# Kernel optimization log

Measured on AMD Instinct MI355X. Metric: run time of the kernel, lower is better.

## Reference

```python
import jax, jax.numpy as jnp
import numpy as np

B, T, D, H, L, V = 2, 1024, 1024, 16, 6, 32000
HD = D // H  # head_size = n_emb // n_heads
EPS = 1e-5   # torch LayerNorm default


def setup_inputs() -> dict:
    key = jax.random.key(0)
    ks = jax.random.split(key, 19)
    s = 0.02
    n = lambda k, shape: jax.random.normal(k, shape, dtype=jnp.float32) * s
    return {
        "idx": jax.random.randint(ks[0], (B, T), 0, V),
        "targets": jax.random.randint(ks[1], (B, T), 0, V),
        "tok_emb": n(ks[2], (V, D)),
        "pos_emb": n(ks[3], (V, D)),  # only first T rows used, as in the source
        "Wq": n(ks[4], (L, H, D, HD)),
        "Wk": n(ks[5], (L, H, D, HD)),
        "Wv": n(ks[6], (L, H, D, HD)),
        "Wo": n(ks[7], (L, D, D)),
        "bo": n(ks[8], (L, D)),
        "W1": n(ks[9], (L, D, 4 * D)),
        "b1": n(ks[10], (L, 4 * D)),
        "W2": n(ks[11], (L, 4 * D, D)),
        "b2": n(ks[12], (L, D)),
        "ln_g": jnp.ones((D,), jnp.float32),
        "ln_b": jnp.zeros((D,), jnp.float32),
        "Wf": n(ks[13], (D, V)),
        "bf": n(ks[14], (V,)),
    }


def _layer_norm(x, g, b):
    mu = jnp.mean(x, axis=-1, keepdims=True)
    var = jnp.mean(jnp.square(x - mu), axis=-1, keepdims=True)
    return (x - mu) * jax.lax.rsqrt(var + EPS) * g + b


def _forward(idx, targets, tok_emb, pos_emb, Wq, Wk, Wv, Wo, bo,
             W1, b1, W2, b2, ln_g, ln_b, Wf, bf):
    x = tok_emb[idx] + pos_emb[:T]  # [B,T,D]
    tril = jnp.tril(jnp.ones((T, T), dtype=bool))
    scale = jnp.asarray(D, x.dtype) ** -0.5  # NOTE: source scales by C=N_EMBED, not head_size

    def block(x, p):
        wq, wk, wv, wo, bo_, w1, b1_, w2, b2_ = p
        q = jnp.einsum('btd,hde->bhte', x, wq)
        k = jnp.einsum('btd,hde->bhte', x, wk)
        v = jnp.einsum('btd,hde->bhte', x, wv)
        scores = jnp.einsum('bhte,bhse->bhts', q, k) * scale
        scores = jnp.where(tril, scores, -jnp.inf)
        att = jax.nn.softmax(scores, axis=-1)
        o = jnp.einsum('bhts,bhse->bhte', att, v)
        o = o.transpose(0, 2, 1, 3).reshape(B, T, D)  # concat heads
        x = x + o @ wo + bo_                           # attn residual (no LN in source)
        h = jax.nn.relu(x @ w1 + b1_)
        x = x + h @ w2 + b2_                           # ffn residual
        return x, None

    x, _ = jax.lax.scan(block, x, (Wq, Wk, Wv, Wo, bo, W1, b1, W2, b2))
    x = _layer_norm(x, ln_g, ln_b)
    logits = x @ Wf + bf  # [B,T,V]
    logp = jax.nn.log_softmax(logits, axis=-1)
    nll = -jnp.take_along_axis(logp, targets[..., None], axis=-1)
    loss = jnp.mean(nll)
    return logits, loss


def reference(idx, targets, tok_emb, pos_emb, Wq, Wk, Wv, Wo, bo,
              W1, b1, W2, b2, ln_g, ln_b, Wf, bf):
    return _forward(idx, targets, tok_emb, pos_emb, Wq, Wk, Wv, Wo, bo,
                    W1, b1, W2, b2, ln_g, ln_b, Wf, bf)
```

## Files before the change

### kernel.cpp

```cpp
#include <hip/hip_runtime.h>
#include <hip/hip_bf16.h>

typedef unsigned short u16;
typedef unsigned int u32;
typedef float f32x4 __attribute__((ext_vector_type(4)));
typedef __bf16 bf16x8 __attribute__((ext_vector_type(8)));

#define NB 2
#define NT 1024
#define ND 1024
#define NH 16
#define HDIM 64
#define NL 6
#define NV 32000
#define ND4 4096
#define BT (NB * NT)
#define L2E 1.44269504f
#define NSLOT 500

__device__ __forceinline__ u16 f2b(float f) {
  u32 u = __builtin_bit_cast(u32, f);
  u32 r = (u + 0x7FFFu + ((u >> 16) & 1u)) >> 16;
  return (u16)r;
}

__device__ __forceinline__ void gl_lds16(const void* g, void* lds) {
  __builtin_amdgcn_global_load_lds((const __attribute__((address_space(1))) u32*)g,
                                   (__attribute__((address_space(3))) u32*)lds, 16, 0, 0);
}

__device__ __forceinline__ float rsum16(float v) {
  v += __shfl_xor(v, 1, 64);
  v += __shfl_xor(v, 2, 64);
  v += __shfl_xor(v, 4, 64);
  v += __shfl_xor(v, 8, 64);
  return v;
}

__device__ __forceinline__ void tr512(const float* in, int in_rs, u16* out, int out_rs,
                                      int k0, int n0, float (*t)[65]) {
  int tid = threadIdx.x;
#pragma unroll
  for (int i = 0; i < 8; ++i) {
    int e = tid + 512 * i;
    int r = e >> 6, c = e & 63;
    t[r][c] = in[(size_t)(k0 + r) * in_rs + n0 + c];
  }
  __syncthreads();
#pragma unroll
  for (int i = 0; i < 8; ++i) {
    int e = tid + 512 * i;
    int r = e >> 6, c = e & 63;
    out[(size_t)(n0 + r) * out_rs + k0 + c] = f2b(t[c][r]);
  }
}

__device__ __forceinline__ void trans512_blk(
    int i, int l, const float* Wq, const float* Wk, const float* Wv,
    const float* Wo, const float* W1, const float* W2,
    u16* wqkvT, u16* woT, u16* w1T, u16* w2T, float (*t)[65]) {
  if (i < 768) {
    int x = i & 15, z = i >> 4;
    int s = z >> 4, h = z & 15;
    const float* in = (s == 0 ? Wq : s == 1 ? Wk : Wv) + ((size_t)(l * NH + h)) * ND * HDIM;
    u16* o = wqkvT + ((size_t)(s * ND + h * HDIM)) * ND;
    tr512(in, HDIM, o, ND, x * 64, 0, t);
  } else if (i < 1024) {
    int j = i - 768, x = j & 15, y = j >> 4;
    tr512(Wo + (size_t)l * ND * ND, ND, woT, ND, y * 64, x * 64, t);
  } else if (i < 2048) {
    int j = i - 1024, x = j & 63, y = j >> 6;
    tr512(W1 + (size_t)l * ND * ND4, ND4, w1T, ND, y * 64, x * 64, t);
  } else {
    int j = i - 2048, x = j & 15, y = j >> 4;
    tr512(W2 + (size_t)l * ND4 * ND, ND, w2T, ND4, y * 64, x * 64, t);
  }
}

__global__ void __launch_bounds__(512) k_pre(const int* __restrict__ idx,
                                             const float* __restrict__ tok,
                                             const float* __restrict__ pos,
                                             float* __restrict__ xf, u16* __restrict__ xb,
                                             const float* __restrict__ Wq,
                                             const float* __restrict__ Wk,
                                             const float* __restrict__ Wv,
                                             const float* __restrict__ Wo,
                                             const float* __restrict__ W1,
                                             const float* __restrict__ W2,
                                             u16* __restrict__ wT0) {
  __shared__ float t[64][65];
  int bid = blockIdx.x;
  if (bid < 1024) {
    int tid = threadIdx.x;
    int row = bid * 2 + (tid >> 8);
    int tt = row & (NT - 1);
    int tk = idx[row];
    int c = (tid & 255) * 4;
    float4 a = *(const float4*)(tok + (size_t)tk * ND + c);
    float4 p = *(const float4*)(pos + (size_t)tt * ND + c);
    float4 s = make_float4(a.x + p.x, a.y + p.y, a.z + p.z, a.w + p.w);
    *(float4*)(xf + (size_t)row * ND + c) = s;
    u16* o = xb + (size_t)row * ND + c;
    *(u32*)(o + 0) = (u32)f2b(s.x) | ((u32)f2b(s.y) << 16);
    *(u32*)(o + 2) = (u32)f2b(s.z) | ((u32)f2b(s.w) << 16);
    return;
  }
  trans512_blk(bid - 1024, 0, Wq, Wk, Wv, Wo, W1, W2,
               wT0, wT0 + (size_t)3 * ND * ND, wT0 + (size_t)4 * ND * ND,
               wT0 + (size_t)8 * ND * ND, t);
}

template <int EPI>
__global__ void __launch_bounds__(512, 2)
k_gemm8(const u16* __restrict__ A, const u16* __restrict__ Bt,
        const float* __restrict__ bias, float* __restrict__ outf,
        u16* __restrict__ outb, int K, int N, int nMt, float* __restrict__ pl) {
  __shared__ u16 lds[2][2][2][128 * 64];
  int tid = threadIdx.x;
  int w = tid >> 6, l = tid & 63;
  int l4 = l >> 4, lm = l & 15;
  int wm = w >> 2, wn = w & 3;

  int nwg = gridDim.x, bid = blockIdx.x;
  int q8 = nwg >> 3, r8 = nwg & 7;
  int xcd = bid & 7, loc = bid >> 3;
  int swz = (xcd < r8 ? xcd * (q8 + 1) : r8 * (q8 + 1) + (xcd - r8) * q8) + loc;
  int m0 = (swz % nMt) * 256;
  int n0 = (swz / nMt) * 256;

  f32x4 acc[8][4];
  f32x4 z = {0.f, 0.f, 0.f, 0.f};
#pragma unroll
  for (int m = 0; m < 8; ++m)
#pragma unroll
    for (int n = 0; n < 4; ++n) acc[m][n] = z;

  int srow = (w << 3) + (l >> 3);
  int scol = (((l & 7) ^ ((l >> 3) & 7)) << 3);
  int sdst = w * 512 + l * 8;

  auto stage_half = [&](int b, int mat, int h, int kt) {
    int k0 = kt << 6;
    const u16* base = (mat == 0 ? A + (size_t)(m0 + (h << 7)) * K
                                : Bt + (size_t)(n0 + (h << 7)) * K);
#pragma unroll
    for (int i = 0; i < 2; ++i)
      gl_lds16(base + (size_t)(i * 64 + srow) * K + k0 + scol,
               &lds[b][mat][h][i * 4096 + sdst]);
  };

  int c0 = (l4 ^ (lm & 7)) * 8;
  int c1 = c0 ^ 32;
  int brow0 = (wn & 1) * 64;

  const u16* A0h = &lds[0][0][wm][0];
  const u16* B0h = &lds[0][1][wn >> 1][0];
  const u16* A1h = &lds[1][0][wm][0];
  const u16* B1h = &lds[1][1][wn >> 1][0];

  bf16x8 Ar[4][2], Bx[2][2], By[2][2];

  auto dsA = [&](const u16* Ah, int mf0) {
#pragma unroll
    for (int mf = 0; mf < 4; ++mf) {
      Ar[mf][0] = *(const bf16x8*)&Ah[((mf0 + mf) * 16 + lm) * 64 + c0];
      Ar[mf][1] = *(const bf16x8*)&Ah[((mf0 + mf) * 16 + lm) * 64 + c1];
    }
  };
  auto dsB = [&](const u16* Bh, bf16x8 (&B)[2][2], int nf0) {
#pragma unroll
    for (int nf = 0; nf < 2; ++nf) {
      B[nf][0] = *(const bf16x8*)&Bh[(brow0 + (nf0 + nf) * 16 + lm) * 64 + c0];
      B[nf][1] = *(const bf16x8*)&Bh[(brow0 + (nf0 + nf) * 16 + lm) * 64 + c1];
    }
  };
  auto mm = [&](int am, bf16x8 (&B)[2][2], int an) {
    __builtin_amdgcn_s_setprio(1);
#pragma unroll
    for (int mf = 0; mf < 4; ++mf)
#pragma unroll
      for (int nf = 0; nf < 2; ++nf) {
        acc[am + mf][an + nf] =
            __builtin_amdgcn_mfma_f32_16x16x32_bf16(Ar[mf][0], B[nf][0], acc[am + mf][an + nf], 0, 0, 0);
        acc[am + mf][an + nf] =
            __builtin_amdgcn_mfma_f32_16x16x32_bf16(Ar[mf][1], B[nf][1], acc[am + mf][an + nf], 0, 0, 0);
      }
    __builtin_amdgcn_s_setprio(0);
  };
  auto openbar = [&]() {
    __builtin_amdgcn_sched_barrier(0);
    __builtin_amdgcn_s_barrier();
    __builtin_amdgcn_sched_barrier(0);
  };
  auto midbar = [&]() {
    __builtin_amdgcn_sched_barrier(0);
    __builtin_amdgcn_s_barrier();
    asm volatile("s_waitcnt lgkmcnt(0)" ::: "memory");
    __builtin_amdgcn_sched_barrier(0);
  };

  int nk = K >> 6;
  stage_half(0, 0, 0, 0); stage_half(0, 0, 1, 0);
  stage_half(0, 1, 0, 0); stage_half(0, 1, 1, 0);
  stage_half(1, 0, 0, 1);

  for (int u = 0; u < nk; u += 2) {
    bool s2 = (u + 2 < nk), s3 = (u + 3 < nk);
    asm volatile("s_waitcnt vmcnt(2)" ::: "memory");
    openbar();
    dsA(A0h, 0); dsB(B0h, Bx, 0);
    stage_half(1, 0, 1, u + 1);
    midbar();
    mm(0, Bx, 0);
    openbar();
    dsB(B0h, By, 2);
    stage_half(1, 1, 0, u + 1);
    midbar();
    mm(0, By, 2);
    openbar();
    dsA(A0h, 4);
    stage_half(1, 1, 1, u + 1);
    midbar();
    mm(4, By, 2);
    openbar();
    if (s2) stage_half(0, 0, 0, u + 2);
    midbar();
    mm(4, Bx, 0);
    if (s2) asm volatile("s_waitcnt vmcnt(2)" ::: "memory");
    else    asm volatile("s_waitcnt vmcnt(0)" ::: "memory");
    openbar();
    dsA(A1h, 0); dsB(B1h, Bx, 0);
    if (s2) stage_half(0, 0, 1, u + 2);
    midbar();
    mm(0, Bx, 0);
    openbar();
    dsB(B1h, By, 2);
    if (s2) stage_half(0, 1, 0, u + 2);
    midbar();
    mm(0, By, 2);
    openbar();
    dsA(A1h, 4);
    if (s2) stage_half(0, 1, 1, u + 2);
    midbar();
    mm(4, By, 2);
    openbar();
    if (s3) stage_half(1, 0, 0, u + 3);
    midbar();
    mm(4, Bx, 0);
  }

  if constexpr (EPI == 4) {
    int slot = (n0 >> 6) + wn;
#pragma unroll
    for (int mf = 0; mf < 8; ++mf)
#pragma unroll
      for (int j = 0; j < 4; ++j) {
        int row = m0 + wm * 128 + mf * 16 + l4 * 4 + j;
        float sm = 0.f;
#pragma unroll
        for (int nf = 0; nf < 4; ++nf) {
          int col = n0 + wn * 64 + nf * 16 + lm;
          float v = acc[mf][nf][j] + bias[col];
          __builtin_nontemporal_store(v, &outf[(size_t)row * N + col]);
          sm += exp2f(v * L2E);
        }
        sm = rsum16(sm);
        if (lm == 0) pl[(size_t)row * NSLOT + slot] = sm;
      }
  } else {
#pragma unroll
    for (int mf = 0; mf < 8; ++mf)
#pragma unroll
      for (int nf = 0; nf < 4; ++nf)
#pragma unroll
        for (int j = 0; j < 4; ++j) {
          int row = m0 + wm * 128 + mf * 16 + l4 * 4 + j;
          int col = n0 + wn * 64 + nf * 16 + lm;
          float v = acc[mf][nf][j];
          if constexpr (EPI == 0) outb[(size_t)row * N + col] = f2b(v);
          else __builtin_nontemporal_store(v + bias[col], &outf[(size_t)row * N + col]);
        }
  }
}

template <int EPI, int BM, int BN>
__global__ void __launch_bounds__(256, BM == 64 ? 4 : (BN == 64 ? 3 : 2))
k_gemm4(const u16* __restrict__ A, const u16* __restrict__ Bt,
        const float* __restrict__ bias, float* __restrict__ outf,
        u16* __restrict__ outb, int K, int N, int nMt) {
  constexpr int NFW = BN / 32;
  constexpr int NH2 = NFW / 2;
  constexpr int AF = BM / 32;
  __shared__ u16 As[2][BM * 64];
  __shared__ u16 Bs[2][BN * 64];
  int tid = threadIdx.x;
  int w = tid >> 6, l = tid & 63;
  int l4 = l >> 4, lm = l & 15;
  int wr = w >> 1, wc = w & 1;

  int nwg = gridDim.x, bid = blockIdx.x;
  int q8 = nwg >> 3, r8 = nwg & 7;
  int xcd = bid & 7, loc = bid >> 3;
  int swz = (xcd < r8 ? xcd * (q8 + 1) : r8 * (q8 + 1) + (xcd - r8) * q8) + loc;
  int m0 = (swz % nMt) * BM;
  int n0 = (swz / nMt) * BN;

  f32x4 acc[AF][NFW];
  f32x4 z = {0.f, 0.f, 0.f, 0.f};
#pragma unroll
  for (int m = 0; m < AF; ++m)
#pragma unroll
    for (int n = 0; n < NFW; ++n) acc[m][n] = z;

  int srow = (w << 3) + (l >> 3);
  int scol = (((l & 7) ^ ((l >> 3) & 7)) << 3);
  int sdst = w * 512 + l * 8;

  const u16* Arow = A + (size_t)m0 * K;
  const u16* Brow = Bt + (size_t)n0 * K;

  auto stage = [&](int b, int kt) {
    int k0 = kt << 6;
#pragma unroll
    for (int i = 0; i < BM / 32; ++i)
      gl_lds16(Arow + (size_t)(i * 32 + srow) * K + k0 + scol, &As[b][i * 2048 + sdst]);
#pragma unroll
    for (int i = 0; i < BN / 32; ++i)
      gl_lds16(Brow + (size_t)(i * 32 + srow) * K + k0 + scol, &Bs[b][i * 2048 + sdst]);
  };

  int c0 = (l4 ^ (lm & 7)) * 8;
  int c1 = c0 ^ 32;

  int nk = K >> 6;
  stage(0, 0);
  for (int t = 0; t < nk; ++t) {
    int b = t & 1;
    asm volatile("s_waitcnt vmcnt(0)" ::: "memory");
    __builtin_amdgcn_sched_barrier(0);
    __builtin_amdgcn_s_barrier();
    __builtin_amdgcn_sched_barrier(0);
    if (t + 1 < nk) stage(b ^ 1, t + 1);
    __builtin_amdgcn_sched_barrier(0);

    bf16x8 af[AF][2], bfr[NH2][2];
#pragma unroll
    for (int mf = 0; mf < AF; ++mf) {
      af[mf][0] = *(const bf16x8*)&As[b][(mf * 16 + lm) * 64 + c0 + wr * (BM / 2) * 64];
      af[mf][1] = *(const bf16x8*)&As[b][(mf * 16 + lm) * 64 + c1 + wr * (BM / 2) * 64];
    }
#pragma unroll
    for (int nf = 0; nf < NH2; ++nf) {
      int brow = wc * (BN / 2) + nf * 16 + lm;
      bfr[nf][0] = *(const bf16x8*)&Bs[b][brow * 64 + c0];
      bfr[nf][1] = *(const bf16x8*)&Bs[b][brow * 64 + c1];
    }
    __builtin_amdgcn_s_setprio(1);
#pragma unroll
    for (int mf = 0; mf < AF; ++mf)
#pragma unroll
      for (int nf = 0; nf < NH2; ++nf) {
        acc[mf][nf] = __builtin_amdgcn_mfma_f32_16x16x32_bf16(af[mf][0], bfr[nf][0], acc[mf][nf], 0, 0, 0);
        acc[mf][nf] = __builtin_amdgcn_mfma_f32_16x16x32_bf16(af[mf][1], bfr[nf][1], acc[mf][nf], 0, 0, 0);
      }
    __builtin_amdgcn_s_setprio(0);

#pragma unroll
    for (int nf = 0; nf < NH2; ++nf) {
      int brow = wc * (BN / 2) + (nf + NH2) * 16 + lm;
      bfr[nf][0] = *(const bf16x8*)&Bs[b][brow * 64 + c0];
      bfr[nf][1] = *(const bf16x8*)&Bs[b][brow * 64 + c1];
    }
    __builtin_amdgcn_s_setprio(1);
#pragma unroll
    for (int mf = 0; mf < AF; ++mf)
#pragma unroll
      for (int nf = 0; nf < NH2; ++nf) {
        acc[mf][nf + NH2] = __builtin_amdgcn_mfma_f32_16x16x32_bf16(af[mf][0], bfr[nf][0], acc[mf][nf + NH2], 0, 0, 0);
        acc[mf][nf + NH2] = __builtin_amdgcn_mfma_f32_16x16x32_bf16(af[mf][1], bfr[nf][1], acc[mf][nf + NH2], 0, 0, 0);
      }
    __builtin_amdgcn_s_setprio(0);
  }

#pragma unroll
  for (int mf = 0; mf < AF; ++mf)
#pragma unroll
    for (int nf = 0; nf < NFW; ++nf)
#pragma unroll
      for (int j = 0; j < 4; ++j) {
        int row = m0 + wr * (BM / 2) + mf * 16 + l4 * 4 + j;
        int col = n0 + wc * (BN / 2) + nf * 16 + lm;
        float v = acc[mf][nf][j];
        if constexpr (EPI == 0) {
          outb[(size_t)row * N + col] = f2b(v);
        } else if constexpr (EPI == 2) {
          v += bias[col];
          outb[(size_t)row * N + col] = f2b(fmaxf(v, 0.f));
        } else {
          v += bias[col];
          size_t o = (size_t)row * N + col;
          float nx = outf[o] + v;
          outf[o] = nx;
          outb[o] = f2b(nx);
        }
      }
}

__global__ void __launch_bounds__(512, 2) k_attn_mega(
    const u16* __restrict__ qkv, u16* __restrict__ ob,
    const float* __restrict__ Wq, const float* __restrict__ Wk,
    const float* __restrict__ Wv, const float* __restrict__ Wo,
    const float* __restrict__ W1, const float* __restrict__ W2,
    const float* __restrict__ Wf, u16* __restrict__ wTnext,
    u16* __restrict__ wfT, int lNext, int wfStart) {
  __shared__ char smem[70656];
  int bid = blockIdx.x;
  if (bid >= 256) {
    auto t = reinterpret_cast<float(*)[65]>(smem);
    int i = bid - 256;
    int nTrans = (lNext < NL) ? 3072 : 0;
    if (i < nTrans) {
      trans512_blk(i, lNext, Wq, Wk, Wv, Wo, W1, W2,
                   wTnext, wTnext + (size_t)3 * ND * ND, wTnext + (size_t)4 * ND * ND,
                   wTnext + (size_t)8 * ND * ND, t);
    } else {
      int j = wfStart + (i - nTrans);
      int x = j % 500, y = j / 500;
      tr512(Wf, NV, wfT, ND, y * 64, x * 64, t);
    }
    return;
  }
  u16* Ks = (u16*)smem;
  u16* Vt = Ks + 128 * 72;
  u16* Pw = Vt + 64 * 136;
  int qb = bid & 7, h = (bid >> 3) & 15, b = bid >> 7;
  int tid = threadIdx.x;
  int w = tid >> 6, l = tid & 63;
  int l4 = l >> 4, lm = l & 15;

  const u16* base = qkv + (size_t)b * NT * 3072 + h * HDIM;
  int r0 = tid >> 3, e0 = (tid & 7) << 3;

  auto loadT = [&](int kb, bf16x8& k0, bf16x8& k1, bf16x8& v0, bf16x8& v1) {
    const u16* s0 = base + (size_t)(kb * 128 + r0) * 3072;
    const u16* s1 = s0 + (size_t)64 * 3072;
    k0 = *(const bf16x8*)(s0 + 1024 + e0);
    v0 = *(const bf16x8*)(s0 + 2048 + e0);
    k1 = *(const bf16x8*)(s1 + 1024 + e0);
    v1 = *(const bf16x8*)(s1 + 2048 + e0);
  };

  f32x4 z = {0.f, 0.f, 0.f, 0.f};

  bf16x8 qf[2];
#pragma unroll
  for (int kk = 0; kk < 2; ++kk) {
    int tq = qb * 128 + w * 16 + lm;
    qf[kk] = *(const bf16x8*)(base + (size_t)tq * 3072 + kk * 32 + l4 * 8);
  }

  f32x4 oacc[4];
  float lrow[4];
#pragma unroll
  for (int n = 0; n < 4; ++n) oacc[n] = z;
#pragma unroll
  for (int j = 0; j < 4; ++j) lrow[j] = 0.f;

  bf16x8 ck0, ck1, cv0, cv1;
  loadT(0, ck0, ck1, cv0, cv1);
  bf16x8 nk0 = ck0, nk1 = ck1, nv0 = cv0, nv1 = cv1;

  for (int kb = 0; kb <= qb; ++kb) {
    __syncthreads();
    {
      *(bf16x8*)&Ks[r0 * 72 + e0] = ck0;
      *(bf16x8*)&Ks[(r0 + 64) * 72 + e0] = ck1;
      union { bf16x8 v; u16 u[8]; } a, c;
      a.v = cv0; c.v = cv1;
#pragma unroll
      for (int j = 0; j < 8; ++j) {
        Vt[(e0 + j) * 136 + r0] = a.u[j];
        Vt[(e0 + j) * 136 + r0 + 64] = c.u[j];
      }
    }
    if (kb < qb) loadT(kb + 1, nk0, nk1, nv0, nv1);
    __syncthreads();

    f32x4 s[8];
#pragma unroll
    for (int n = 0; n < 8; ++n) s[n] = z;
#pragma unroll
    for (int kk = 0; kk < 2; ++kk)
#pragma unroll
      for (int n = 0; n < 8; ++n) {
        bf16x8 kf = *(const bf16x8*)&Ks[(n * 16 + lm) * 72 + kk * 32 + l4 * 8];
        s[n] = __builtin_amdgcn_mfma_f32_16x16x32_bf16(qf[kk], kf, s[n], 0, 0, 0);
      }

    bool diag = (kb == qb);
#pragma unroll
    for (int j = 0; j < 4; ++j) {
      int rloc = w * 16 + l4 * 4 + j;
      int prow = l4 * 4 + j;
      float rs = 0.f;
#pragma unroll
      for (int n = 0; n < 8; ++n) {
        float p = exp2f(s[n][j] * (0.03125f * L2E));
        if (diag && (n * 16 + lm > rloc)) p = 0.f;
        rs += p;
        Pw[(w * 16 + prow) * 136 + n * 16 + lm] = f2b(p);
      }
      lrow[j] += rs;
    }
    asm volatile("s_waitcnt lgkmcnt(0)" ::: "memory");
    __builtin_amdgcn_sched_barrier(0);

#pragma unroll
    for (int kk = 0; kk < 4; ++kk) {
      bf16x8 pa = *(const bf16x8*)&Pw[(w * 16 + lm) * 136 + kk * 32 + l4 * 8];
#pragma unroll
      for (int n = 0; n < 4; ++n) {
        bf16x8 vf = *(const bf16x8*)&Vt[(n * 16 + lm) * 136 + kk * 32 + l4 * 8];
        oacc[n] = __builtin_amdgcn_mfma_f32_16x16x32_bf16(pa, vf, oacc[n], 0, 0, 0);
      }
    }

    ck0 = nk0; ck1 = nk1; cv0 = nv0; cv1 = nv1;
  }

#pragma unroll
  for (int j = 0; j < 4; ++j) lrow[j] = rsum16(lrow[j]);

#pragma unroll
  for (int n = 0; n < 4; ++n)
#pragma unroll
    for (int j = 0; j < 4; ++j) {
      int tq = qb * 128 + w * 16 + l4 * 4 + j;
      int col = h * HDIM + n * 16 + lm;
      float v = oacc[n][j] / lrow[j];
      ob[(size_t)(b * NT + tq) * ND + col] = f2b(v);
    }
}

__global__ void k_ln(const float* __restrict__ xf, const float* __restrict__ g,
                     const float* __restrict__ bta, u16* __restrict__ xb) {
  __shared__ float red[4];
  int row = blockIdx.x, tid = threadIdx.x;
  int w = tid >> 6;
  int c = tid * 4;
  float4 x = *(const float4*)(xf + (size_t)row * ND + c);
  float s = x.x + x.y + x.z + x.w;
#pragma unroll
  for (int off = 1; off < 64; off <<= 1) s += __shfl_xor(s, off, 64);
  if ((tid & 63) == 0) red[w] = s;
  __syncthreads();
  float mu = (red[0] + red[1] + red[2] + red[3]) * (1.0f / ND);
  float d0 = x.x - mu, d1 = x.y - mu, d2 = x.z - mu, d3 = x.w - mu;
  float v = d0 * d0 + d1 * d1 + d2 * d2 + d3 * d3;
  __syncthreads();
#pragma unroll
  for (int off = 1; off < 64; off <<= 1) v += __shfl_xor(v, off, 64);
  if ((tid & 63) == 0) red[w] = v;
  __syncthreads();
  float var = (red[0] + red[1] + red[2] + red[3]) * (1.0f / ND);
  float rs = rsqrtf(var + 1e-5f);
  float4 gg = *(const float4*)(g + c);
  float4 bb = *(const float4*)(bta + c);
  u16* o = xb + (size_t)row * ND + c;
  o[0] = f2b(d0 * rs * gg.x + bb.x);
  o[1] = f2b(d1 * rs * gg.y + bb.y);
  o[2] = f2b(d2 * rs * gg.z + bb.z);
  o[3] = f2b(d3 * rs * gg.w + bb.w);
}

__global__ void k_loss_row2(const float* __restrict__ pl, const float* __restrict__ logits,
                            const int* __restrict__ tgt, float* __restrict__ lossbuf) {
  int row = blockIdx.x, l = threadIdx.x;
  const float* pr = pl + (size_t)row * NSLOT;
  float s = 0.f;
  for (int i = l; i < NSLOT; i += 64) s += pr[i];
#pragma unroll
  for (int off = 1; off < 64; off <<= 1) s += __shfl_xor(s, off, 64);
  if (l == 0) lossbuf[row] = logf(s) - logits[(size_t)row * NV + tgt[row]];
}

__global__ void k_loss_final(const float* __restrict__ lossbuf, float* __restrict__ out) {
  __shared__ float red[4];
  int tid = threadIdx.x;
  float s = 0.f;
  for (int i = tid; i < BT; i += 256) s += lossbuf[i];
#pragma unroll
  for (int off = 1; off < 64; off <<= 1) s += __shfl_xor(s, off, 64);
  if ((tid & 63) == 0) red[tid >> 6] = s;
  __syncthreads();
  if (tid == 0) out[0] = (red[0] + red[1] + red[2] + red[3]) * (1.0f / BT);
}

extern "C" void kernel_launch(void* const* d_in, const int* in_sizes, int n_in,
                              void* d_out, int out_size, void* d_ws, size_t ws_size,
                              hipStream_t stream) {
  const int* idx = (const int*)d_in[0];
  const int* tgt = (const int*)d_in[1];
  const float* tok = (const float*)d_in[2];
  const float* pos = (const float*)d_in[3];
  const float* Wq = (const float*)d_in[4];
  const float* Wk = (const float*)d_in[5];
  const float* Wv = (const float*)d_in[6];
  const float* Wo = (const float*)d_in[7];
  const float* bo = (const float*)d_in[8];
  const float* W1 = (const float*)d_in[9];
  const float* b1 = (const float*)d_in[10];
  const float* W2 = (const float*)d_in[11];
  const float* b2 = (const float*)d_in[12];
  const float* lng = (const float*)d_in[13];
  const float* lnb = (const float*)d_in[14];
  const float* Wf = (const float*)d_in[15];
  const float* bfp = (const float*)d_in[16];
  float* logits = (float*)d_out;
  float* lossp = logits + (size_t)BT * NV;

  char* ws = (char*)d_ws;
  u16* wT0 = (u16*)ws;
  u16* wT1 = wT0 + (size_t)12 * ND * ND;
  u16* wfT = wT1 + (size_t)12 * ND * ND;
  size_t off = (size_t)24 * ND * ND * 2 + (size_t)NV * ND * 2;
  float* xf = (float*)(ws + off); off += (size_t)BT * ND * 4;
  u16* xb = (u16*)(ws + off);     off += (size_t)BT * ND * 2;
  u16* qkv = (u16*)(ws + off);    off += (size_t)BT * 3 * ND * 2;
  u16* obuf = (u16*)(ws + off);   off += (size_t)BT * ND * 2;
  u16* hb = (u16*)(ws + off);     off += (size_t)BT * ND4 * 2;
  float* pl = (float*)(ws + off); off += (size_t)BT * NSLOT * 4;
  float* lossbuf = (float*)(ws + off);

  k_pre<<<4096, 512, 0, stream>>>(idx, tok, pos, xf, xb, Wq, Wk, Wv, Wo, W1, W2, wT0);
  int wfDone = 0;
  for (int l = 0; l < NL; ++l) {
    u16* wTl = (l & 1) ? wT1 : wT0;
    u16* wTn = (l & 1) ? wT0 : wT1;
    u16* wqkvT = wTl;
    u16* woT = wTl + (size_t)3 * ND * ND;
    u16* w1T = wTl + (size_t)4 * ND * ND;
    u16* w2T = wTl + (size_t)8 * ND * ND;
    k_gemm4<0, 128, 128><<<384, 256, 0, stream>>>(xb, wqkvT, nullptr, nullptr, qkv, ND, 3 * ND, 16);
    int nTrans = (l + 1 < NL) ? 3072 : 0;
    int wfCount = (l + 1 < NL) ? 1333 : (8000 - wfDone);
    k_attn_mega<<<256 + nTrans + wfCount, 512, 0, stream>>>(
        qkv, obuf, Wq, Wk, Wv, Wo, W1, W2, Wf, wTn, wfT, l + 1, wfDone);
    wfDone += wfCount;
    k_gemm4<3, 64, 64><<<512, 256, 0, stream>>>(obuf, woT, bo + (size_t)l * ND, xf, xb, ND, ND, 32);
    k_gemm4<2, 128, 128><<<512, 256, 0, stream>>>(xb, w1T, b1 + (size_t)l * ND4, nullptr, hb, ND, ND4, 16);
    k_gemm4<3, 64, 64><<<512, 256, 0, stream>>>(hb, w2T, b2 + (size_t)l * ND, xf, xb, ND4, ND, 32);
  }
  k_ln<<<BT, 256, 0, stream>>>(xf, lng, lnb, xb);
  k_gemm8<4><<<1000, 512, 0, stream>>>(xb, wfT, bfp, logits, nullptr, ND, NV, 8, pl);
  k_loss_row2<<<BT, 64, 0, stream>>>(pl, logits, tgt, lossbuf);
  k_loss_final<<<1, 256, 0, stream>>>(lossbuf, lossp);
}
```

Baseline: 1.071 ms.

## Emit transposed V from QKV GEMM and read K/V directly from global in attention

The QKV projection GEMM gains an epilogue that also writes V in a per-head transposed layout. The attention kernel then drops its LDS staging of K and V, along with its syncthreads and register prefetch, and loads MFMA fragments directly from global memory. LDS use per block shrinks, which may allow more blocks per CU. The cost is extra scattered stores in the GEMM epilogue and uncached, latency-exposed global loads inside the attention inner loop, with no prefetch to hide them.

Measured after the change: 1.336 ms. 1.25x slower.

```diff
diff --git a/kernel.cpp b/kernel.cpp
--- a/kernel.cpp
+++ b/kernel.cpp
@@ -287,7 +287,7 @@
 __global__ void __launch_bounds__(256, BM == 64 ? 4 : (BN == 64 ? 3 : 2))
 k_gemm4(const u16* __restrict__ A, const u16* __restrict__ Bt,
         const float* __restrict__ bias, float* __restrict__ outf,
-        u16* __restrict__ outb, int K, int N, int nMt) {
+        u16* __restrict__ outb, int K, int N, int nMt, u16* __restrict__ vt) {
   constexpr int NFW = BN / 32;
   constexpr int NH2 = NFW / 2;
   constexpr int AF = BM / 32;
@@ -391,8 +391,13 @@
         int row = m0 + wr * (BM / 2) + mf * 16 + l4 * 4 + j;
         int col = n0 + wc * (BN / 2) + nf * 16 + lm;
         float v = acc[mf][nf][j];
-        if constexpr (EPI == 0) {
-          outb[(size_t)row * N + col] = f2b(v);
+        if constexpr (EPI == 0 || EPI == 5) {
+          u16 bv = f2b(v);
+          outb[(size_t)row * N + col] = bv;
+          if constexpr (EPI == 5) {
+            if (col >= 2048)
+              vt[((size_t)((row >> 10) * 1024 + col - 2048) << 10) | (row & 1023)] = bv;
+          }
         } else if constexpr (EPI == 2) {
           v += bias[col];
           outb[(size_t)row * N + col] = f2b(fmaxf(v, 0.f));
@@ -407,13 +412,13 @@
 }
 
 __global__ void __launch_bounds__(512, 2) k_attn_mega(
-    const u16* __restrict__ qkv, u16* __restrict__ ob,
+    const u16* __restrict__ qkv, const u16* __restrict__ vT, u16* __restrict__ ob,
     const float* __restrict__ Wq, const float* __restrict__ Wk,
     const float* __restrict__ Wv, const float* __restrict__ Wo,
     const float* __restrict__ W1, const float* __restrict__ W2,
     const float* __restrict__ Wf, u16* __restrict__ wTnext,
     u16* __restrict__ wfT, int lNext, int wfStart) {
-  __shared__ char smem[70656];
+  __shared__ char smem[34816];
   int bid = blockIdx.x;
   if (bid >= 256) {
     auto t = reinterpret_cast<float(*)[65]>(smem);
@@ -430,25 +435,14 @@
     }
     return;
   }
-  u16* Ks = (u16*)smem;
-  u16* Vt = Ks + 128 * 72;
-  u16* Pw = Vt + 64 * 136;
+  u16* Pw = (u16*)smem;
   int qb = bid & 7, h = (bid >> 3) & 15, b = bid >> 7;
   int tid = threadIdx.x;
   int w = tid >> 6, l = tid & 63;
   int l4 = l >> 4, lm = l & 15;
 
   const u16* base = qkv + (size_t)b * NT * 3072 + h * HDIM;
-  int r0 = tid >> 3, e0 = (tid & 7) << 3;
-
-  auto loadT = [&](int kb, bf16x8& k0, bf16x8& k1, bf16x8& v0, bf16x8& v1) {
-    const u16* s0 = base + (size_t)(kb * 128 + r0) * 3072;
-    const u16* s1 = s0 + (size_t)64 * 3072;
-    k0 = *(const bf16x8*)(s0 + 1024 + e0);
-    v0 = *(const bf16x8*)(s0 + 2048 + e0);
-    k1 = *(const bf16x8*)(s1 + 1024 + e0);
-    v1 = *(const bf16x8*)(s1 + 2048 + e0);
-  };
+  const u16* vbase = vT + ((size_t)(b * NH + h) << 16);
 
   f32x4 z = {0.f, 0.f, 0.f, 0.f};
 
@@ -466,26 +460,7 @@
 #pragma unroll
   for (int j = 0; j < 4; ++j) lrow[j] = 0.f;
 
-  bf16x8 ck0, ck1, cv0, cv1;
-  loadT(0, ck0, ck1, cv0, cv1);
-  bf16x8 nk0 = ck0, nk1 = ck1, nv0 = cv0, nv1 = cv1;
-
   for (int kb = 0; kb <= qb; ++kb) {
-    __syncthreads();
-    {
-      *(bf16x8*)&Ks[r0 * 72 + e0] = ck0;
-      *(bf16x8*)&Ks[(r0 + 64) * 72 + e0] = ck1;
-      union { bf16x8 v; u16 u[8]; } a, c;
-      a.v = cv0; c.v = cv1;
-#pragma unroll
-      for (int j = 0; j < 8; ++j) {
-        Vt[(e0 + j) * 136 + r0] = a.u[j];
-        Vt[(e0 + j) * 136 + r0 + 64] = c.u[j];
-      }
-    }
-    if (kb < qb) loadT(kb + 1, nk0, nk1, nv0, nv1);
-    __syncthreads();
-
     f32x4 s[8];
 #pragma unroll
     for (int n = 0; n < 8; ++n) s[n] = z;
@@ -493,7 +468,8 @@
     for (int kk = 0; kk < 2; ++kk)
 #pragma unroll
       for (int n = 0; n < 8; ++n) {
-        bf16x8 kf = *(const bf16x8*)&Ks[(n * 16 + lm) * 72 + kk * 32 + l4 * 8];
+        bf16x8 kf = *(const bf16x8*)(base + (size_t)(kb * 128 + n * 16 + lm) * 3072 +
+                                     1024 + kk * 32 + l4 * 8);
         s[n] = __builtin_amdgcn_mfma_f32_16x16x32_bf16(qf[kk], kf, s[n], 0, 0, 0);
       }
 
@@ -520,12 +496,12 @@
       bf16x8 pa = *(const bf16x8*)&Pw[(w * 16 + lm) * 136 + kk * 32 + l4 * 8];
 #pragma unroll
       for (int n = 0; n < 4; ++n) {
-        bf16x8 vf = *(const bf16x8*)&Vt[(n * 16 + lm) * 136 + kk * 32 + l4 * 8];
+        bf16x8 vf = *(const bf16x8*)(vbase + ((size_t)(n * 16 + lm) << 10) +
+                                     kb * 128 + kk * 32 + l4 * 8);
         oacc[n] = __builtin_amdgcn_mfma_f32_16x16x32_bf16(pa, vf, oacc[n], 0, 0, 0);
       }
     }
-
-    ck0 = nk0; ck1 = nk1; cv0 = nv0; cv1 = nv1;
+    __builtin_amdgcn_sched_barrier(0);
   }
 
 #pragma unroll
@@ -627,6 +603,7 @@
   float* xf = (float*)(ws + off); off += (size_t)BT * ND * 4;
   u16* xb = (u16*)(ws + off);     off += (size_t)BT * ND * 2;
   u16* qkv = (u16*)(ws + off);    off += (size_t)BT * 3 * ND * 2;
+  u16* vTb = (u16*)(ws + off);    off += (size_t)NB * NH * HDIM * NT * 2;
   u16* obuf = (u16*)(ws + off);   off += (size_t)BT * ND * 2;
   u16* hb = (u16*)(ws + off);     off += (size_t)BT * ND4 * 2;
   float* pl = (float*)(ws + off); off += (size_t)BT * NSLOT * 4;
@@ -641,15 +618,15 @@
     u16* woT = wTl + (size_t)3 * ND * ND;
     u16* w1T = wTl + (size_t)4 * ND * ND;
     u16* w2T = wTl + (size_t)8 * ND * ND;
-    k_gemm4<0, 128, 128><<<384, 256, 0, stream>>>(xb, wqkvT, nullptr, nullptr, qkv, ND, 3 * ND, 16);
+    k_gemm4<5, 128, 128><<<384, 256, 0, stream>>>(xb, wqkvT, nullptr, nullptr, qkv, ND, 3 * ND, 16, vTb);
     int nTrans = (l + 1 < NL) ? 3072 : 0;
     int wfCount = (l + 1 < NL) ? 1333 : (8000 - wfDone);
     k_attn_mega<<<256 + nTrans + wfCount, 512, 0, stream>>>(
-        qkv, obuf, Wq, Wk, Wv, Wo, W1, W2, Wf, wTn, wfT, l + 1, wfDone);
+        qkv, vTb, obuf, Wq, Wk, Wv, Wo, W1, W2, Wf, wTn, wfT, l + 1, wfDone);
     wfDone += wfCount;
-    k_gemm4<3, 64, 64><<<512, 256, 0, stream>>>(obuf, woT, bo + (size_t)l * ND, xf, xb, ND, ND, 32);
-    k_gemm4<2, 128, 128><<<512, 256, 0, stream>>>(xb, w1T, b1 + (size_t)l * ND4, nullptr, hb, ND, ND4, 16);
-    k_gemm4<3, 64, 64><<<512, 256, 0, stream>>>(hb, w2T, b2 + (size_t)l * ND, xf, xb, ND4, ND, 32);
+    k_gemm4<3, 64, 64><<<512, 256, 0, stream>>>(obuf, woT, bo + (size_t)l * ND, xf, xb, ND, ND, 32, nullptr);
+    k_gemm4<2, 128, 128><<<512, 256, 0, stream>>>(xb, w1T, b1 + (size_t)l * ND4, nullptr, hb, ND, ND4, 16, nullptr);
+    k_gemm4<3, 64, 64><<<512, 256, 0, stream>>>(hb, w2T, b2 + (size_t)l * ND, xf, xb, ND4, ND, 32, nullptr);
   }
   k_ln<<<BT, 256, 0, stream>>>(xf, lng, lnb, xb);
   k_gemm8<4><<<1000, 512, 0, stream>>>(xb, wfT, bfp, logits, nullptr, ND, NV, 8, pl);
```
